# Optimization experiments

Hardware: AMD Instinct MI355X
Metric: run time of the kernel (lower is better)

Reference implementation:

```python
import jax, jax.numpy as jnp
import numpy as np

B, S, CTXD, QD, ATTD = 32, 4096, 512, 512, 256

def setup_inputs() -> dict:
    key = jax.random.key(0)
    ks = jax.random.split(key, 7)
    qry = jax.random.normal(ks[0], (B, QD), dtype=jnp.float32)
    ctx = jax.random.normal(ks[1], (B, S, CTXD), dtype=jnp.float32)
    ctx_mask = jax.random.randint(ks[2], (B, S), 0, 2, dtype=jnp.int32)
    # ensure no all-zero row (would make softmax NaN)
    ctx_mask = ctx_mask.at[:, 0].set(1)
    sc = 1.0 / np.sqrt(CTXD + QD)
    W = jax.random.uniform(ks[3], (CTXD + QD, ATTD), jnp.float32, -sc, sc)
    b = jax.random.uniform(ks[4], (ATTD,), jnp.float32, -sc, sc)
    sc2 = 1.0 / np.sqrt(ATTD)
    w2 = jax.random.uniform(ks[5], (ATTD, 1), jnp.float32, -sc2, sc2)
    b2 = jax.random.uniform(ks[6], (1,), jnp.float32, -sc2, sc2)
    return {"qry": qry, "ctx": ctx, "ctx_mask": ctx_mask, "W": W, "b": b, "w2": w2, "b2": b2}

def reference(qry, ctx, ctx_mask, W, b, w2, b2):
    # cat([ctx, qry_rep]) @ W == ctx @ W_ctx + qry @ W_qry ; avoids the [B,S,ctxdim+qdim] concat
    W_ctx, W_qry = W[:CTXD], W[CTXD:]
    h = jnp.einsum('bsc,ca->bsa', ctx, W_ctx) + (qry @ W_qry)[:, None, :] + b  # [B,S,ATTD]
    y = jnp.tanh(h)
    scores = jnp.einsum('bsa,a->bs', y, w2[:, 0]) + b2[0]  # [B,S]
    scores = scores + jnp.log(ctx_mask.astype(jnp.float32))
    alphas = jax.nn.softmax(scores, axis=-1)  # [B,S]
    summary = jnp.einsum('bsc,bs->bc', ctx, alphas)  # [B,CTXD]
    return (alphas, summary, scores)
```

## Files before the change

kernel.cpp:

```cpp
#include <hip/hip_runtime.h>
#include <math.h>

#define B_ 32
#define S_ 4096
#define CTXD_ 512
#define QD_ 512
#define ATTD_ 256

#define RT 64
#define NCH (S_ / RT)

#define MASKED_SCORE (-1e30f)

#define AOFF0 0
#define AOFF1 5120
#define BOFF0 10240
#define BOFF1 30720
#define LDS_BYTES 51200

typedef __attribute__((ext_vector_type(8))) short bf16x8;
typedef __attribute__((ext_vector_type(4))) float f32x4;

__device__ __forceinline__ unsigned short f2bf(float f) {
    unsigned u = __float_as_uint(f);
    u += 0x7fff + ((u >> 16) & 1);
    return (unsigned short)(u >> 16);
}
__device__ __forceinline__ unsigned pk2(float lo, float hi) {
    return (unsigned)f2bf(lo) | ((unsigned)f2bf(hi) << 16);
}

__device__ __forceinline__ float fast_tanh(float x) {
    float xc = fminf(fmaxf(x, -15.f), 15.f);
    float t = __expf(2.f * xc);
    return (t - 1.f) / (t + 1.f);
}

__global__ __launch_bounds__(256) void prep_kernel(
    const float* __restrict__ W, const float* __restrict__ qry,
    const float* __restrict__ bias, unsigned short* __restrict__ Wt,
    float* __restrict__ qh) {
    __shared__ unsigned char lds[64 * 66 * 2];
    const int bid = blockIdx.x;
    const int t = threadIdx.x;
    if (bid < 32) {
        unsigned short(*tile)[66] = (unsigned short(*)[66])lds;
        const int kk = (bid >> 2) * 64;
        const int nn = (bid & 3) * 64;
        #pragma unroll
        for (int i = 0; i < 4; ++i) {
            const int r = i * 16 + (t >> 4);
            float4 v = ((const float4*)(W + (size_t)(kk + r) * ATTD_ + nn))[t & 15];
            unsigned short* tr = &tile[r][(t & 15) * 4];
            tr[0] = f2bf(v.x); tr[1] = f2bf(v.y);
            tr[2] = f2bf(v.z); tr[3] = f2bf(v.w);
        }
        __syncthreads();
        const int l8 = (t & 7) * 8;
        #pragma unroll
        for (int p = 0; p < 2; ++p) {
            const int n = p * 32 + (t >> 3);
            uint4 o;
            o.x = (unsigned)tile[l8 + 0][n] | ((unsigned)tile[l8 + 1][n] << 16);
            o.y = (unsigned)tile[l8 + 2][n] | ((unsigned)tile[l8 + 3][n] << 16);
            o.z = (unsigned)tile[l8 + 4][n] | ((unsigned)tile[l8 + 5][n] << 16);
            o.w = (unsigned)tile[l8 + 6][n] | ((unsigned)tile[l8 + 7][n] << 16);
            *(uint4*)(Wt + (size_t)(nn + n) * CTXD_ + kk + l8) = o;
        }
    } else {
        float* q = (float*)lds;
        const int b = bid - 32;
        for (int i = t; i < QD_; i += 256) q[i] = qry[b * QD_ + i];
        __syncthreads();
        float acc = bias[t];
        const float* Wq = W + (size_t)CTXD_ * ATTD_ + t;
        #pragma unroll 8
        for (int k = 0; k < QD_; ++k) acc += q[k] * Wq[(size_t)k * ATTD_];
        qh[b * ATTD_ + t] = acc;
    }
}

__global__ __launch_bounds__(256, 3) void scores_kernel(
    const float* __restrict__ ctx, const unsigned short* __restrict__ Wt,
    const float* __restrict__ qh, const float* __restrict__ w2,
    const float* __restrict__ b2, const int* __restrict__ mask,
    float* __restrict__ scores, float* __restrict__ mstat,
    float* __restrict__ lstat, float* __restrict__ part) {
    __shared__ __attribute__((aligned(16))) unsigned char lds[LDS_BYTES];
    const int t = threadIdx.x;
    const int b = blockIdx.y;
    const int ch = blockIdx.x;
    const int s0 = ch * RT;
    const int tx = t & 63;
    const int w = t >> 6;
    const int wm = w & 1;
    const int wn = w >> 1;
    const int frow = tx & 15;
    const int fq = tx >> 4;

    f32x4 c00, c01, c02, c03, c04, c05, c06, c07;
    f32x4 c10, c11, c12, c13, c14, c15, c16, c17;
    c00 = c01 = c02 = c03 = c04 = c05 = c06 = c07 = (f32x4)0.f;
    c10 = c11 = c12 = c13 = c14 = c15 = c16 = c17 = (f32x4)0.f;

    const float* ctxb = ctx + ((size_t)b * S_ + s0) * CTXD_;
    const int arow = t >> 2;
    const int akq = t & 3;
    const int bn = t;

    float4 fa0_0, fa1_0, fa0_1, fa1_1;
    uint4 pb0_0, pb1_0, pb2_0, pb3_0;
    uint4 pb0_1, pb1_1, pb2_1, pb3_1;

#define ISSUE(S, kk)                                                         \
    {                                                                        \
        const float* ap = ctxb + (size_t)arow * CTXD_ + (kk) * 32 + akq * 8; \
        fa0_##S = ((const float4*)ap)[0];                                    \
        fa1_##S = ((const float4*)ap)[1];                                    \
        const uint4* bp = (const uint4*)(Wt + (size_t)bn * CTXD_ + (kk) * 32); \
        pb0_##S = bp[0]; pb1_##S = bp[1]; pb2_##S = bp[2]; pb3_##S = bp[3];  \
    }
#define WRITE(S, P)                                                          \
    {                                                                        \
        uint4 wv;                                                            \
        wv.x = pk2(fa0_##S.x, fa0_##S.y); wv.y = pk2(fa0_##S.z, fa0_##S.w);  \
        wv.z = pk2(fa1_##S.x, fa1_##S.y); wv.w = pk2(fa1_##S.z, fa1_##S.w);  \
        *(uint4*)(lds + AOFF##P + arow * 80 + akq * 16) = wv;                \
        uint4* bw = (uint4*)(lds + BOFF##P + bn * 80);                       \
        bw[0] = pb0_##S; bw[1] = pb1_##S; bw[2] = pb2_##S; bw[3] = pb3_##S;  \
    }
#define MM1(ni, P)                                                           \
    {                                                                        \
        bf16x8 bf = *(const bf16x8*)(lds + BOFF##P +                         \
                                     (wn * 128 + (ni) * 16 + frow) * 80 +    \
                                     fq * 16);                               \
        c0##ni = __builtin_amdgcn_mfma_f32_16x16x32_bf16(a0, bf, c0##ni, 0, 0, 0); \
        c1##ni = __builtin_amdgcn_mfma_f32_16x16x32_bf16(a1, bf, c1##ni, 0, 0, 0); \
    }
#define COMPUTE(P)                                                           \
    {                                                                        \
        const unsigned char* aB = lds + AOFF##P + (wm * 32 + frow) * 80 + fq * 16; \
        bf16x8 a0 = *(const bf16x8*)aB;                                      \
        bf16x8 a1 = *(const bf16x8*)(aB + 16 * 80);                          \
        MM1(0, P) MM1(1, P) MM1(2, P) MM1(3, P)                              \
        MM1(4, P) MM1(5, P) MM1(6, P) MM1(7, P)                              \
    }
#define BAR                                                                  \
    asm volatile("s_waitcnt lgkmcnt(0)" ::: "memory");                       \
    __builtin_amdgcn_s_barrier();                                            \
    __builtin_amdgcn_sched_barrier(0);

    ISSUE(0, 0) ISSUE(1, 1)
    WRITE(0, 0) ISSUE(0, 2)
    BAR
    WRITE(1, 1) ISSUE(1, 3)  COMPUTE(0) BAR
    WRITE(0, 0) ISSUE(0, 4)  COMPUTE(1) BAR
    WRITE(1, 1) ISSUE(1, 5)  COMPUTE(0) BAR
    WRITE(0, 0) ISSUE(0, 6)  COMPUTE(1) BAR
    WRITE(1, 1) ISSUE(1, 7)  COMPUTE(0) BAR
    WRITE(0, 0) ISSUE(0, 8)  COMPUTE(1) BAR
    WRITE(1, 1) ISSUE(1, 9)  COMPUTE(0) BAR
    WRITE(0, 0) ISSUE(0, 10) COMPUTE(1) BAR
    WRITE(1, 1) ISSUE(1, 11) COMPUTE(0) BAR
    WRITE(0, 0) ISSUE(0, 12) COMPUTE(1) BAR
    WRITE(1, 1) ISSUE(1, 13) COMPUTE(0) BAR
    WRITE(0, 0) ISSUE(0, 14) COMPUTE(1) BAR
    WRITE(1, 1) ISSUE(1, 15) COMPUTE(0) BAR
    WRITE(0, 0)              COMPUTE(1) BAR
    WRITE(1, 1)              COMPUTE(0) BAR
    COMPUTE(1)
#undef BAR
#undef COMPUTE
#undef MM1
#undef WRITE
#undef ISSUE

    const float* qhb = qh + b * ATTD_ + wn * 128;
    const float* w2b = w2 + wn * 128;
    float p00 = 0.f, p01 = 0.f, p02 = 0.f, p03 = 0.f;
    float p10 = 0.f, p11 = 0.f, p12 = 0.f, p13 = 0.f;
#define EPI(ni)                                                              \
    {                                                                        \
        float qv = qhb[(ni) * 16 + frow];                                    \
        float wv = w2b[(ni) * 16 + frow];                                    \
        p00 += fast_tanh(c0##ni[0] + qv) * wv;                               \
        p01 += fast_tanh(c0##ni[1] + qv) * wv;                               \
        p02 += fast_tanh(c0##ni[2] + qv) * wv;                               \
        p03 += fast_tanh(c0##ni[3] + qv) * wv;                               \
        p10 += fast_tanh(c1##ni[0] + qv) * wv;                               \
        p11 += fast_tanh(c1##ni[1] + qv) * wv;                               \
        p12 += fast_tanh(c1##ni[2] + qv) * wv;                               \
        p13 += fast_tanh(c1##ni[3] + qv) * wv;                               \
    }
    EPI(0) EPI(1) EPI(2) EPI(3) EPI(4) EPI(5) EPI(6) EPI(7)
#undef EPI
    #pragma unroll
    for (int off = 1; off <= 8; off <<= 1) {
        p00 += __shfl_xor(p00, off, 64);
        p01 += __shfl_xor(p01, off, 64);
        p02 += __shfl_xor(p02, off, 64);
        p03 += __shfl_xor(p03, off, 64);
        p10 += __shfl_xor(p10, off, 64);
        p11 += __shfl_xor(p11, off, 64);
        p12 += __shfl_xor(p12, off, 64);
        p13 += __shfl_xor(p13, off, 64);
    }
    float* sred = (float*)lds;
    float* wl = (float*)(lds + 512);
    float4* pbuf = (float4*)(lds + 1024);
    __syncthreads();
    if (frow == 0) {
        const int base = wn * 64 + wm * 32 + fq * 4;
        sred[base + 0] = p00; sred[base + 1] = p01;
        sred[base + 2] = p02; sred[base + 3] = p03;
        sred[base + 16 + 0] = p10; sred[base + 16 + 1] = p11;
        sred[base + 16 + 2] = p12; sred[base + 16 + 3] = p13;
    }
    __syncthreads();
    if (t < 64) {
        const int s = s0 + t;
        float sc = sred[t] + sred[64 + t] + b2[0];
        const bool msk = (mask[b * S_ + s] == 0);
        if (msk) sc = MASKED_SCORE;
        scores[b * S_ + s] = sc;
        float mloc = sc;
        #pragma unroll
        for (int off = 1; off < 64; off <<= 1)
            mloc = fmaxf(mloc, __shfl_xor(mloc, off, 64));
        const float ws = msk ? 0.f : __expf(sc - mloc);
        float lloc = ws;
        #pragma unroll
        for (int off = 1; off < 64; off <<= 1)
            lloc += __shfl_xor(lloc, off, 64);
        if (t == 0) {
            mstat[b * NCH + ch] = mloc;
            lstat[b * NCH + ch] = lloc;
        }
        wl[t] = ws;
    }
    __syncthreads();
    const int col = t & 63;
    const int q = t >> 6;
    float4 alo = make_float4(0.f, 0.f, 0.f, 0.f);
    float4 ahi = make_float4(0.f, 0.f, 0.f, 0.f);
    #pragma unroll 4
    for (int s = q; s < RT; s += 4) {
        const float al = wl[s];
        const float4* row = (const float4*)(ctxb + (size_t)s * CTXD_);
        float4 v0 = row[col];
        float4 v1 = row[col + 64];
        alo.x += v0.x * al; alo.y += v0.y * al;
        alo.z += v0.z * al; alo.w += v0.w * al;
        ahi.x += v1.x * al; ahi.y += v1.y * al;
        ahi.z += v1.z * al; ahi.w += v1.w * al;
    }
    pbuf[q * 128 + col] = alo;
    pbuf[q * 128 + col + 64] = ahi;
    __syncthreads();
    if (t < 128) {
        float4 a0 = pbuf[t], a1 = pbuf[128 + t], a2 = pbuf[256 + t], a3 = pbuf[384 + t];
        float4 r;
        r.x = a0.x + a1.x + a2.x + a3.x;
        r.y = a0.y + a1.y + a2.y + a3.y;
        r.z = a0.z + a1.z + a2.z + a3.z;
        r.w = a0.w + a1.w + a2.w + a3.w;
        ((float4*)(part + ((size_t)(b * NCH + ch)) * CTXD_))[t] = r;
    }
}

__global__ __launch_bounds__(256) void combine_kernel(
    const float* __restrict__ mstat, const float* __restrict__ lstat,
    const float* __restrict__ part, const float* __restrict__ scores,
    float* __restrict__ alphas, float* __restrict__ summary) {
    const int b = blockIdx.y, seg = blockIdx.x, t = threadIdx.x;
    __shared__ float e[NCH];
    __shared__ float gstat[2];
    if (t < NCH) {
        const float mi = mstat[b * NCH + t];
        const float li = lstat[b * NCH + t];
        float m = mi;
        #pragma unroll
        for (int off = 1; off < 64; off <<= 1)
            m = fmaxf(m, __shfl_xor(m, off, 64));
        const float ei = __expf(mi - m);
        float l = ei * li;
        #pragma unroll
        for (int off = 1; off < 64; off <<= 1)
            l += __shfl_xor(l, off, 64);
        e[t] = ei;
        if (t == 0) { gstat[0] = m; gstat[1] = 1.0f / l; }
    }
    __syncthreads();
    const float m = gstat[0], il = gstat[1];
    const int c4 = t & 31;
    const int grp = t >> 5;
    float4 acc = make_float4(0.f, 0.f, 0.f, 0.f);
    for (int chv = grp; chv < NCH; chv += 8) {
        const float ei = e[chv];
        float4 v =
            ((const float4*)(part + ((size_t)(b * NCH + chv)) * CTXD_ + seg * 128))[c4];
        acc.x += ei * v.x; acc.y += ei * v.y;
        acc.z += ei * v.z; acc.w += ei * v.w;
    }
    __shared__ float4 buf[8][32];
    buf[grp][c4] = acc;
    __syncthreads();
    if (t < 32) {
        float4 r = make_float4(0.f, 0.f, 0.f, 0.f);
        #pragma unroll
        for (int g = 0; g < 8; ++g) {
            float4 v = buf[g][t];
            r.x += v.x; r.y += v.y; r.z += v.z; r.w += v.w;
        }
        r.x *= il; r.y *= il; r.z *= il; r.w *= il;
        ((float4*)(summary + (size_t)b * CTXD_ + seg * 128))[t] = r;
    }
    const int sbase = seg * 1024;
    #pragma unroll
    for (int i = 0; i < 4; ++i) {
        const int s = sbase + i * 256 + t;
        alphas[b * S_ + s] = __expf(scores[b * S_ + s] - m) * il;
    }
}

extern "C" void kernel_launch(void* const* d_in, const int* in_sizes, int n_in,
                              void* d_out, int out_size, void* d_ws,
                              size_t ws_size, hipStream_t stream) {
    const float* qry = (const float*)d_in[0];
    const float* ctx = (const float*)d_in[1];
    const int* mask = (const int*)d_in[2];
    const float* W = (const float*)d_in[3];
    const float* bias = (const float*)d_in[4];
    const float* w2 = (const float*)d_in[5];
    const float* b2 = (const float*)d_in[6];

    float* out = (float*)d_out;
    float* alphas = out;
    float* summary = out + B_ * S_;
    float* scores = out + B_ * S_ + B_ * CTXD_;

    unsigned short* Wt = (unsigned short*)d_ws;
    float* qh = (float*)((char*)d_ws + (size_t)ATTD_ * CTXD_ * 2);
    float* mstat = qh + B_ * ATTD_;
    float* lstat = mstat + B_ * NCH;
    float* part = lstat + B_ * NCH;

    prep_kernel<<<64, 256, 0, stream>>>(W, qry, bias, Wt, qh);
    scores_kernel<<<dim3(NCH, B_), 256, 0, stream>>>(ctx, Wt, qh, w2, b2, mask,
                                                     scores, mstat, lstat, part);
    combine_kernel<<<dim3(4, B_), 256, 0, stream>>>(mstat, lstat, part, scores,
                                                    alphas, summary);
}
```

Measured before the change: 476.5 us.

## Load weight tiles directly into LDS via global_load_lds with k-tiled layout

Prep now writes the bf16 weight in a k-tile-major linear layout, so each 32-wide k slice is one contiguous 16KB block. The scores kernel copies that block straight into LDS with global_load_lds instead of staging it through registers. This removes the VGPR round-trip and lets the LDS footprint shrink (row stride 64 bytes instead of 80). The pipeline is reworked into a single-buffer-register scheme with two __syncthreads per step. The unpadded 64-byte stride may cause LDS bank conflicts on the B-fragment reads, and the prefetch depth drops from two stages to one.

New measurement: 461.8 us. -3.1%, faster.

```diff
diff --git a/kernel.cpp b/kernel.cpp
--- a/kernel.cpp
+++ b/kernel.cpp
@@ -15,8 +15,8 @@
 #define AOFF0 0
 #define AOFF1 5120
 #define BOFF0 10240
-#define BOFF1 30720
-#define LDS_BYTES 51200
+#define BOFF1 26624
+#define LDS_BYTES 43008
 
 typedef __attribute__((ext_vector_type(8))) short bf16x8;
 typedef __attribute__((ext_vector_type(4))) float f32x4;
@@ -38,7 +38,7 @@
 
 __global__ __launch_bounds__(256) void prep_kernel(
     const float* __restrict__ W, const float* __restrict__ qry,
-    const float* __restrict__ bias, unsigned short* __restrict__ Wt,
+    const float* __restrict__ bias, unsigned short* __restrict__ Wt_lin,
     float* __restrict__ qh) {
     __shared__ unsigned char lds[64 * 66 * 2];
     const int bid = blockIdx.x;
@@ -56,16 +56,18 @@
             tr[2] = f2bf(v.z); tr[3] = f2bf(v.w);
         }
         __syncthreads();
-        const int l8 = (t & 7) * 8;
-        #pragma unroll
-        for (int p = 0; p < 2; ++p) {
-            const int n = p * 32 + (t >> 3);
+        const int kt0 = (bid >> 2) * 2;
+        const int n = t & 63;
+        const int q = t >> 6;
+        #pragma unroll
+        for (int kt_loc = 0; kt_loc < 2; ++kt_loc) {
+            const int kbase = kt_loc * 32 + q * 8;
             uint4 o;
-            o.x = (unsigned)tile[l8 + 0][n] | ((unsigned)tile[l8 + 1][n] << 16);
-            o.y = (unsigned)tile[l8 + 2][n] | ((unsigned)tile[l8 + 3][n] << 16);
-            o.z = (unsigned)tile[l8 + 4][n] | ((unsigned)tile[l8 + 5][n] << 16);
-            o.w = (unsigned)tile[l8 + 6][n] | ((unsigned)tile[l8 + 7][n] << 16);
-            *(uint4*)(Wt + (size_t)(nn + n) * CTXD_ + kk + l8) = o;
+            o.x = (unsigned)tile[kbase + 0][n] | ((unsigned)tile[kbase + 1][n] << 16);
+            o.y = (unsigned)tile[kbase + 2][n] | ((unsigned)tile[kbase + 3][n] << 16);
+            o.z = (unsigned)tile[kbase + 4][n] | ((unsigned)tile[kbase + 5][n] << 16);
+            o.w = (unsigned)tile[kbase + 6][n] | ((unsigned)tile[kbase + 7][n] << 16);
+            *(uint4*)(Wt_lin + ((size_t)(kt0 + kt_loc) * 256 + nn + n) * 32 + q * 8) = o;
         }
     } else {
         float* q = (float*)lds;
@@ -81,7 +83,7 @@
 }
 
 __global__ __launch_bounds__(256, 3) void scores_kernel(
-    const float* __restrict__ ctx, const unsigned short* __restrict__ Wt,
+    const float* __restrict__ ctx, const unsigned short* __restrict__ Wt_lin,
     const float* __restrict__ qh, const float* __restrict__ w2,
     const float* __restrict__ b2, const int* __restrict__ mask,
     float* __restrict__ scores, float* __restrict__ mstat,
@@ -106,33 +108,41 @@
     const float* ctxb = ctx + ((size_t)b * S_ + s0) * CTXD_;
     const int arow = t >> 2;
     const int akq = t & 3;
-    const int bn = t;
-
-    float4 fa0_0, fa1_0, fa0_1, fa1_1;
-    uint4 pb0_0, pb1_0, pb2_0, pb3_0;
-    uint4 pb0_1, pb1_1, pb2_1, pb3_1;
-
-#define ISSUE(S, kk)                                                         \
+
+    const unsigned char* wtl =
+        (const unsigned char*)Wt_lin + w * 4096 + tx * 16;
+
+    float4 fa0, fa1;
+
+#define ISSUE_A(kt)                                                          \
     {                                                                        \
-        const float* ap = ctxb + (size_t)arow * CTXD_ + (kk) * 32 + akq * 8; \
-        fa0_##S = ((const float4*)ap)[0];                                    \
-        fa1_##S = ((const float4*)ap)[1];                                    \
-        const uint4* bp = (const uint4*)(Wt + (size_t)bn * CTXD_ + (kk) * 32); \
-        pb0_##S = bp[0]; pb1_##S = bp[1]; pb2_##S = bp[2]; pb3_##S = bp[3];  \
-    }
-#define WRITE(S, P)                                                          \
-    {                                                                        \
-        uint4 wv;                                                            \
-        wv.x = pk2(fa0_##S.x, fa0_##S.y); wv.y = pk2(fa0_##S.z, fa0_##S.w);  \
-        wv.z = pk2(fa1_##S.x, fa1_##S.y); wv.w = pk2(fa1_##S.z, fa1_##S.w);  \
-        *(uint4*)(lds + AOFF##P + arow * 80 + akq * 16) = wv;                \
-        uint4* bw = (uint4*)(lds + BOFF##P + bn * 80);                       \
-        bw[0] = pb0_##S; bw[1] = pb1_##S; bw[2] = pb2_##S; bw[3] = pb3_##S;  \
+        const float* ap = ctxb + (size_t)arow * CTXD_ + (kt) * 32 + akq * 8; \
+        fa0 = ((const float4*)ap)[0];                                        \
+        fa1 = ((const float4*)ap)[1];                                        \
+    }
+#define ISSUE_B(P, kt)                                                      \
+    {                                                                       \
+        _Pragma("unroll")                                                   \
+        for (int i = 0; i < 4; ++i) {                                       \
+            __builtin_amdgcn_global_load_lds(                               \
+                (const __attribute__((address_space(1))) unsigned int*)     \
+                    (wtl + (kt) * 16384 + i * 1024),                        \
+                (__attribute__((address_space(3))) unsigned int*)           \
+                    (lds + BOFF##P + w * 4096 + i * 1024),                  \
+                16, 0, 0);                                                  \
+        }                                                                   \
+    }
+#define WRITE_A(P)                                                          \
+    {                                                                       \
+        uint4 wv;                                                           \
+        wv.x = pk2(fa0.x, fa0.y); wv.y = pk2(fa0.z, fa0.w);                 \
+        wv.z = pk2(fa1.x, fa1.y); wv.w = pk2(fa1.z, fa1.w);                 \
+        *(uint4*)(lds + AOFF##P + arow * 80 + akq * 16) = wv;               \
     }
 #define MM1(ni, P)                                                           \
     {                                                                        \
         bf16x8 bf = *(const bf16x8*)(lds + BOFF##P +                         \
-                                     (wn * 128 + (ni) * 16 + frow) * 80 +    \
+                                     (wn * 128 + (ni) * 16 + frow) * 64 +    \
                                      fq * 16);                               \
         c0##ni = __builtin_amdgcn_mfma_f32_16x16x32_bf16(a0, bf, c0##ni, 0, 0, 0); \
         c1##ni = __builtin_amdgcn_mfma_f32_16x16x32_bf16(a1, bf, c1##ni, 0, 0, 0); \
@@ -145,35 +155,28 @@
         MM1(0, P) MM1(1, P) MM1(2, P) MM1(3, P)                              \
         MM1(4, P) MM1(5, P) MM1(6, P) MM1(7, P)                              \
     }
-#define BAR                                                                  \
-    asm volatile("s_waitcnt lgkmcnt(0)" ::: "memory");                       \
-    __builtin_amdgcn_s_barrier();                                            \
-    __builtin_amdgcn_sched_barrier(0);
-
-    ISSUE(0, 0) ISSUE(1, 1)
-    WRITE(0, 0) ISSUE(0, 2)
-    BAR
-    WRITE(1, 1) ISSUE(1, 3)  COMPUTE(0) BAR
-    WRITE(0, 0) ISSUE(0, 4)  COMPUTE(1) BAR
-    WRITE(1, 1) ISSUE(1, 5)  COMPUTE(0) BAR
-    WRITE(0, 0) ISSUE(0, 6)  COMPUTE(1) BAR
-    WRITE(1, 1) ISSUE(1, 7)  COMPUTE(0) BAR
-    WRITE(0, 0) ISSUE(0, 8)  COMPUTE(1) BAR
-    WRITE(1, 1) ISSUE(1, 9)  COMPUTE(0) BAR
-    WRITE(0, 0) ISSUE(0, 10) COMPUTE(1) BAR
-    WRITE(1, 1) ISSUE(1, 11) COMPUTE(0) BAR
-    WRITE(0, 0) ISSUE(0, 12) COMPUTE(1) BAR
-    WRITE(1, 1) ISSUE(1, 13) COMPUTE(0) BAR
-    WRITE(0, 0) ISSUE(0, 14) COMPUTE(1) BAR
-    WRITE(1, 1) ISSUE(1, 15) COMPUTE(0) BAR
-    WRITE(0, 0)              COMPUTE(1) BAR
-    WRITE(1, 1)              COMPUTE(0) BAR
+#define STEP(P, PN, k)                                                      \
+    __syncthreads();                                                        \
+    WRITE_A(P)                                                              \
+    __syncthreads();                                                        \
+    ISSUE_B(PN, (k) + 1) ISSUE_A((k) + 1)                                   \
+    COMPUTE(P)
+
+    ISSUE_B(0, 0) ISSUE_A(0)
+    STEP(0, 1, 0)  STEP(1, 0, 1)  STEP(0, 1, 2)  STEP(1, 0, 3)
+    STEP(0, 1, 4)  STEP(1, 0, 5)  STEP(0, 1, 6)  STEP(1, 0, 7)
+    STEP(0, 1, 8)  STEP(1, 0, 9)  STEP(0, 1, 10) STEP(1, 0, 11)
+    STEP(0, 1, 12) STEP(1, 0, 13) STEP(0, 1, 14)
+    __syncthreads();
+    WRITE_A(1)
+    __syncthreads();
     COMPUTE(1)
-#undef BAR
+#undef STEP
 #undef COMPUTE
 #undef MM1
-#undef WRITE
-#undef ISSUE
+#undef WRITE_A
+#undef ISSUE_B
+#undef ISSUE_A
 
     const float* qhb = qh + b * ATTD_ + wn * 128;
     const float* w2b = w2 + wn * 128;
@@ -339,15 +342,16 @@
     float* summary = out + B_ * S_;
     float* scores = out + B_ * S_ + B_ * CTXD_;
 
-    unsigned short* Wt = (unsigned short*)d_ws;
+    unsigned short* Wt_lin = (unsigned short*)d_ws;
     float* qh = (float*)((char*)d_ws + (size_t)ATTD_ * CTXD_ * 2);
     float* mstat = qh + B_ * ATTD_;
     float* lstat = mstat + B_ * NCH;
     float* part = lstat + B_ * NCH;
 
-    prep_kernel<<<64, 256, 0, stream>>>(W, qry, bias, Wt, qh);
-    scores_kernel<<<dim3(NCH, B_), 256, 0, stream>>>(ctx, Wt, qh, w2, b2, mask,
-                                                     scores, mstat, lstat, part);
+    prep_kernel<<<64, 256, 0, stream>>>(W, qry, bias, Wt_lin, qh);
+    scores_kernel<<<dim3(NCH, B_), 256, 0, stream>>>(ctx, Wt_lin, qh, w2, b2,
+                                                     mask, scores, mstat, lstat,
+                                                     part);
     combine_kernel<<<dim3(4, B_), 256, 0, stream>>>(mstat, lstat, part, scores,
                                                     alphas, summary);
 }
```
